# Optimization experiments

Hardware: AMD Instinct MI355X
Metric: run time of the kernel (lower is better)

The kernel has to match this reference:

```python
import jax, jax.numpy as jnp
import numpy as np

N_NODES = 200_000
N_EDGES = 400_000
EMB_DIM = 128
HID_DIM = 24
N_TYPES = 8


def setup_inputs() -> dict:
    key = jax.random.key(0)
    k_emb, k_src, k_typ, k_w1, k_w2 = jax.random.split(key, 5)
    rgcn_emb = jax.random.normal(k_emb, (N_NODES, EMB_DIM), dtype=jnp.float32)
    edge_index = jax.random.randint(k_src, (2, N_EDGES), 0, N_NODES, dtype=jnp.int32)
    edge_type = jax.random.randint(k_typ, (N_EDGES,), 0, N_TYPES, dtype=jnp.int32)
    # per-edge-type 2-layer MLP params: Linear(2D->H), Linear(H->1)
    W1 = jax.random.normal(k_w1, (N_TYPES, 2 * EMB_DIM, HID_DIM), dtype=jnp.float32) * 0.05
    b1 = jnp.zeros((N_TYPES, HID_DIM), dtype=jnp.float32)
    W2 = jax.random.normal(k_w2, (N_TYPES, HID_DIM), dtype=jnp.float32) * 0.05
    b2 = jnp.zeros((N_TYPES,), dtype=jnp.float32)
    return {"rgcn_emb": rgcn_emb, "edge_index": edge_index, "edge_type": edge_type,
            "W1": W1, "b1": b1, "W2": W2, "b2": b2}


def reference(rgcn_emb, edge_index, edge_type, W1, b1, W2, b2):
    src, dst = edge_index[0], edge_index[1]
    # gather + concat: [E, 2D]
    edge_emb = jnp.concatenate([rgcn_emb[src], rgcn_emb[dst]], axis=-1)
    # dense per-type expert compute, then select by routing (MoE-style)
    h = jnp.einsum('ed,tdh->teh', edge_emb, W1) + b1[:, None, :]  # [T,E,H]
    h = jnp.where(h > 0, h, 0.01 * h)  # LeakyReLU(0.01)
    s = jnp.einsum('teh,th->te', h, W2) + b2[:, None]  # [T,E]
    onehot = jax.nn.one_hot(edge_type, N_TYPES, dtype=s.dtype)  # [E,T]
    scores = jnp.einsum('te,et->e', s, onehot)  # scatter-select per edge
    return (scores, rgcn_emb)
```

## Files before the change

### kernel.cpp

```cpp
#include <hip/hip_runtime.h>


typedef _Float16 h2 __attribute__((ext_vector_type(2)));
typedef float    f4 __attribute__((ext_vector_type(4)));

constexpr int N_NODES = 200000;
constexpr int N_EDGES = 400000;
constexpr int EMB_DIM = 128;
constexpr int HID     = 24;
constexpr int N_TYPES = 8;
constexpr int BLK     = 256;

constexpr int MAX_PAD      = N_EDGES + N_TYPES * (BLK - 1);
constexpr int SCORE_BLOCKS = (MAX_PAD + BLK - 1) / BLK;
constexpr int SC_BLOCKS    = 128;
constexpr int SC_CH        = (N_EDGES + SC_BLOCKS - 1) / SC_BLOCKS;

constexpr int PREP_HIST   = 64;
constexpr int PREP_W1     = 16;
constexpr int PREP_CONV   = 1968;
constexpr int PREP_BLOCKS = PREP_HIST + PREP_W1 + PREP_CONV;

constexpr size_t SORT_BYTES  = (size_t)(16 + MAX_PAD) * sizeof(int);
constexpr size_t EMB16_OFF   = (SORT_BYTES + 255) & ~(size_t)255;
constexpr size_t EMB16_BYTES = (size_t)N_NODES * EMB_DIM * 2;
constexpr size_t W16_OFF     = EMB16_OFF + EMB16_BYTES;
constexpr size_t W16_BYTES   = (size_t)N_TYPES * 128 * HID * 4;
constexpr size_t NEED16      = W16_OFF + W16_BYTES;

__device__ __forceinline__ float fdot2f(h2 a, h2 b, float c) {
#if __has_builtin(__builtin_amdgcn_fdot2)
    return __builtin_amdgcn_fdot2(a, b, c, false);
#else
    return c + (float)a[0] * (float)b[0] + (float)a[1] * (float)b[1];
#endif
}

__global__ __launch_bounds__(BLK) void prep_k(
        const int* __restrict__ etype, int* __restrict__ counts,
        const float* __restrict__ emb, float* __restrict__ out,
        int2* __restrict__ emb16, const float* __restrict__ W1,
        h2* __restrict__ w16) {
    int b = blockIdx.x;
    if (b < PREP_HIST) {
        __shared__ int lc[N_TYPES];
        if (threadIdx.x < N_TYPES) lc[threadIdx.x] = 0;
        __syncthreads();
        const int4* et4 = (const int4*)etype;
        for (int g = b * BLK + threadIdx.x; g < N_EDGES / 4; g += PREP_HIST * BLK) {
            int4 v = et4[g];
            atomicAdd(&lc[v.x], 1); atomicAdd(&lc[v.y], 1);
            atomicAdd(&lc[v.z], 1); atomicAdd(&lc[v.w], 1);
        }
        __syncthreads();
        if (threadIdx.x < N_TYPES) {
            int v = lc[threadIdx.x];
            if (v) atomicAdd(&counts[threadIdx.x], v);
        }
    } else if (b < PREP_HIST + PREP_W1) {
        int cb = b - PREP_HIST;
        for (int p = cb * BLK + threadIdx.x; p < N_TYPES * 128 * HID; p += PREP_W1 * BLK) {
            int t   = p / (128 * HID);
            int rem = p - t * 128 * HID;
            int kp  = rem / HID, j = rem - kp * HID;
            h2 v;
            v[0] = (_Float16)W1[(t * 256 + 2 * kp)     * HID + j];
            v[1] = (_Float16)W1[(t * 256 + 2 * kp + 1) * HID + j];
            w16[p] = v;
        }
    } else {
        int cb = b - PREP_HIST - PREP_W1;
        const f4* in4 = (const f4*)emb;
        f4* o4 = (f4*)(out + N_EDGES);
        const int n4 = N_NODES * EMB_DIM / 4;
        for (int i = cb * BLK + threadIdx.x; i < n4; i += PREP_CONV * BLK) {
            f4 a = __builtin_nontemporal_load(&in4[i]);
            __builtin_nontemporal_store(a, &o4[i]);
            union { int2 v; h2 h[2]; } u;
            u.h[0] = h2{(_Float16)a.x, (_Float16)a.y};
            u.h[1] = h2{(_Float16)a.z, (_Float16)a.w};
            emb16[i] = u.v;
        }
    }
}

__global__ __launch_bounds__(BLK) void scatter_k(
        const int* __restrict__ etype, int* __restrict__ counts,
        int* __restrict__ sorted) {
    __shared__ int lc[N_TYPES], base[N_TYPES];
    int b = blockIdx.x;
    if (threadIdx.x < N_TYPES) lc[threadIdx.x] = 0;
    __syncthreads();
    int e0 = b * SC_CH, e1 = min(e0 + SC_CH, N_EDGES);
    for (int e = e0 + threadIdx.x; e < e1; e += BLK)
        atomicAdd(&lc[etype[e]], 1);
    __syncthreads();
    if (threadIdx.x < N_TYPES)
        base[threadIdx.x] = atomicAdd(&counts[8 + threadIdx.x], lc[threadIdx.x]);
    __syncthreads();
    if (threadIdx.x < N_TYPES) lc[threadIdx.x] = 0;
    __syncthreads();
    int poff[N_TYPES];
    int off = 0;
#pragma unroll
    for (int t = 0; t < N_TYPES; ++t) {
        poff[t] = off;
        off += ((counts[t] + BLK - 1) / BLK) * BLK;
    }
    for (int e = e0 + threadIdx.x; e < e1; e += BLK) {
        int t = etype[e];
        int r = atomicAdd(&lc[t], 1);
        sorted[poff[t] + base[t] + r] = e;
    }
}

__device__ __forceinline__ void compute_chunk(const int4* __restrict__ r,
                                              const h2* __restrict__ wrow,
                                              float acc[HID]) {
    const h2* hp = (const h2*)r;
#pragma unroll
    for (int kp = 0; kp < 32; ++kp) {
#pragma unroll
        for (int j = 0; j < HID; ++j)
            acc[j] = fdot2f(hp[kp], wrow[kp * HID + j], acc[j]);
    }
}

__global__ __launch_bounds__(BLK) void score16_ns_k(
        const unsigned short* __restrict__ emb16u,
        const int* __restrict__ srci, const int* __restrict__ dsti,
        const int* __restrict__ counts, const int* __restrict__ sorted,
        const h2* __restrict__ w16, const float* __restrict__ b1,
        const float* __restrict__ W2, const float* __restrict__ b2,
        float* __restrict__ out) {
    int poff[N_TYPES];
    int off = 0;
#pragma unroll
    for (int t = 0; t < N_TYPES; ++t) {
        poff[t] = off;
        off += ((counts[t] + BLK - 1) / BLK) * BLK;
    }
    int slot0 = blockIdx.x * BLK;
    if (slot0 >= off) return;
    int t = 0;
#pragma unroll
    for (int i = 1; i < N_TYPES; ++i)
        if (slot0 >= poff[i]) t = i;
    t = __builtin_amdgcn_readfirstlane(t);
    int cnt = counts[t];
    int local = slot0 - poff[t] + (int)threadIdx.x;
    if (local >= cnt) return;
    int e = sorted[slot0 + threadIdx.x];
    int s = srci[e], d = dsti[e];

    float acc[HID];
#pragma unroll
    for (int j = 0; j < HID; ++j) acc[j] = b1[t * HID + j];
    const h2* wt = w16 + (size_t)t * 128 * HID;
    const int4* x0 = (const int4*)(emb16u + (size_t)s * EMB_DIM);
    const int4* x1 = (const int4*)(emb16u + (size_t)d * EMB_DIM);

    int4 A[8], B[8];
#pragma unroll
    for (int k = 0; k < 8; ++k) A[k] = x0[k];
#pragma unroll
    for (int k = 0; k < 8; ++k) B[k] = x0[8 + k];
    compute_chunk(A, wt + 0 * 32 * HID, acc);
#pragma unroll
    for (int k = 0; k < 8; ++k) A[k] = x1[k];
    compute_chunk(B, wt + 1 * 32 * HID, acc);
#pragma unroll
    for (int k = 0; k < 8; ++k) B[k] = x1[8 + k];
    compute_chunk(A, wt + 2 * 32 * HID, acc);
    compute_chunk(B, wt + 3 * 32 * HID, acc);

    float sc = b2[t];
#pragma unroll
    for (int j = 0; j < HID; ++j) {
        float h = acc[j];
        h = (h > 0.f) ? h : 0.01f * h;
        sc = fmaf(h, W2[t * HID + j], sc);
    }
    out[e] = sc;
}

__global__ __launch_bounds__(BLK) void fallback_k(
        const float* __restrict__ emb,
        const int* __restrict__ srci, const int* __restrict__ dsti,
        const int* __restrict__ etype,
        const float* __restrict__ W1, const float* __restrict__ b1,
        const float* __restrict__ W2, const float* __restrict__ b2,
        float* __restrict__ out) {
    long long i0 = (long long)blockIdx.x * BLK + threadIdx.x;
    const float4* s4 = (const float4*)emb;
    float4* o4 = (float4*)(out + N_EDGES);
    const long long n4 = (long long)N_NODES * EMB_DIM / 4;
    for (long long i = i0; i < n4; i += (long long)gridDim.x * BLK)
        o4[i] = s4[i];
    for (int e = (int)i0; e < N_EDGES; e += gridDim.x * BLK) {
        int t = etype[e];
        int s = srci[e], d = dsti[e];
        float acc[HID];
#pragma unroll
        for (int j = 0; j < HID; ++j) acc[j] = b1[t * HID + j];
        const float* w = W1 + (size_t)t * 2 * EMB_DIM * HID;
        for (int k = 0; k < EMB_DIM; ++k) {
            float x = emb[(size_t)s * EMB_DIM + k];
#pragma unroll
            for (int j = 0; j < HID; ++j) acc[j] = fmaf(x, w[k * HID + j], acc[j]);
        }
        for (int k = 0; k < EMB_DIM; ++k) {
            float x = emb[(size_t)d * EMB_DIM + k];
#pragma unroll
            for (int j = 0; j < HID; ++j) acc[j] = fmaf(x, w[(EMB_DIM + k) * HID + j], acc[j]);
        }
        float sc = b2[t];
#pragma unroll
        for (int j = 0; j < HID; ++j) {
            float h = acc[j];
            h = (h > 0.f) ? h : 0.01f * h;
            sc = fmaf(h, W2[t * HID + j], sc);
        }
        out[e] = sc;
    }
}

extern "C" void kernel_launch(void* const* d_in, const int* in_sizes, int n_in,
                              void* d_out, int out_size, void* d_ws, size_t ws_size,
                              hipStream_t stream) {
    const float* emb   = (const float*)d_in[0];
    const int*   eidx  = (const int*)d_in[1];
    const int*   etype = (const int*)d_in[2];
    const float* W1    = (const float*)d_in[3];
    const float* b1    = (const float*)d_in[4];
    const float* W2    = (const float*)d_in[5];
    const float* b2    = (const float*)d_in[6];
    float* out = (float*)d_out;
    const int* srci = eidx;
    const int* dsti = eidx + N_EDGES;

    if (ws_size >= NEED16) {
        int* counts = (int*)d_ws;
        int* sorted = counts + 16;
        int2* emb16 = (int2*)((char*)d_ws + EMB16_OFF);
        h2*   w16   = (h2*)((char*)d_ws + W16_OFF);
        (void)hipMemsetAsync(counts, 0, 16 * sizeof(int), stream);
        prep_k<<<PREP_BLOCKS, BLK, 0, stream>>>(etype, counts, emb, out, emb16, W1, w16);
        scatter_k<<<SC_BLOCKS, BLK, 0, stream>>>(etype, counts, sorted);
        score16_ns_k<<<SCORE_BLOCKS, BLK, 0, stream>>>(
            (const unsigned short*)emb16, srci, dsti, counts, sorted,
            w16, b1, W2, b2, out);
    } else {
        fallback_k<<<2048, BLK, 0, stream>>>(emb, srci, dsti, etype, W1, b1, W2, b2, out);
    }
}
```

Baseline: 287.0 us.

## Replace multi-kernel pipeline with cooperative persistent megakernel and fp32 compute

Merges histogram, prefix, scatter and scoring into one cooperative kernel that uses grid syncs, and falls back to four separate launches if the cooperative launch fails. It drops the fp16 conversion of the embedding table and W1, so the per-edge MLP now reads fp32 embeddings and weights directly with fmaf. The memset goes away by replacing the atomic global counts with a per-chunk count table and a deterministic prefix sum. This saves launch overhead and the fp16 conversion pass, at the cost of twice the gather bandwidth per edge, fp32 math instead of dot2, and grid-sync latency.

```diff
diff --git a/kernel.cpp b/kernel.cpp
--- a/kernel.cpp
+++ b/kernel.cpp
@@ -1,8 +1,10 @@
 #include <hip/hip_runtime.h>
-
-
-typedef _Float16 h2 __attribute__((ext_vector_type(2)));
-typedef float    f4 __attribute__((ext_vector_type(4)));
+#include <hip/hip_cooperative_groups.h>
+
+
+namespace cg = cooperative_groups;
+
+typedef float f4 __attribute__((ext_vector_type(4)));
 
 constexpr int N_NODES = 200000;
 constexpr int N_EDGES = 400000;
@@ -11,178 +13,194 @@
 constexpr int N_TYPES = 8;
 constexpr int BLK     = 256;
 
-constexpr int MAX_PAD      = N_EDGES + N_TYPES * (BLK - 1);
+constexpr int CHUNKS  = 128;
+constexpr int CH_SZ   = N_EDGES / CHUNKS;
+constexpr int MAX_PAD = N_EDGES + N_TYPES * (BLK - 1);
 constexpr int SCORE_BLOCKS = (MAX_PAD + BLK - 1) / BLK;
-constexpr int SC_BLOCKS    = 128;
-constexpr int SC_CH        = (N_EDGES + SC_BLOCKS - 1) / SC_BLOCKS;
-
-constexpr int PREP_HIST   = 64;
-constexpr int PREP_W1     = 16;
-constexpr int PREP_CONV   = 1968;
-constexpr int PREP_BLOCKS = PREP_HIST + PREP_W1 + PREP_CONV;
-
-constexpr size_t SORT_BYTES  = (size_t)(16 + MAX_PAD) * sizeof(int);
-constexpr size_t EMB16_OFF   = (SORT_BYTES + 255) & ~(size_t)255;
-constexpr size_t EMB16_BYTES = (size_t)N_NODES * EMB_DIM * 2;
-constexpr size_t W16_OFF     = EMB16_OFF + EMB16_BYTES;
-constexpr size_t W16_BYTES   = (size_t)N_TYPES * 128 * HID * 4;
-constexpr size_t NEED16      = W16_OFF + W16_BYTES;
-
-__device__ __forceinline__ float fdot2f(h2 a, h2 b, float c) {
-#if __has_builtin(__builtin_amdgcn_fdot2)
-    return __builtin_amdgcn_fdot2(a, b, c, false);
-#else
-    return c + (float)a[0] * (float)b[0] + (float)a[1] * (float)b[1];
-#endif
-}
-
-__global__ __launch_bounds__(BLK) void prep_k(
-        const int* __restrict__ etype, int* __restrict__ counts,
-        const float* __restrict__ emb, float* __restrict__ out,
-        int2* __restrict__ emb16, const float* __restrict__ W1,
-        h2* __restrict__ w16) {
-    int b = blockIdx.x;
-    if (b < PREP_HIST) {
+
+constexpr int OFF_COUNTS = 0;
+constexpr int OFF_POFF   = 8;
+constexpr int OFF_CC     = 16;
+constexpr int OFF_BASE   = OFF_CC + CHUNKS * N_TYPES;
+constexpr int OFF_SORTED = OFF_BASE + CHUNKS * N_TYPES;
+constexpr size_t WS_INTS = (size_t)OFF_SORTED + MAX_PAD;
+
+
+__device__ __forceinline__ void phaseA(int b, int G,
+        const int* __restrict__ etype, const float* __restrict__ emb,
+        float* __restrict__ out, int* __restrict__ ws) {
+    if (b < CHUNKS) {
         __shared__ int lc[N_TYPES];
         if (threadIdx.x < N_TYPES) lc[threadIdx.x] = 0;
         __syncthreads();
-        const int4* et4 = (const int4*)etype;
-        for (int g = b * BLK + threadIdx.x; g < N_EDGES / 4; g += PREP_HIST * BLK) {
-            int4 v = et4[g];
-            atomicAdd(&lc[v.x], 1); atomicAdd(&lc[v.y], 1);
-            atomicAdd(&lc[v.z], 1); atomicAdd(&lc[v.w], 1);
-        }
-        __syncthreads();
-        if (threadIdx.x < N_TYPES) {
-            int v = lc[threadIdx.x];
-            if (v) atomicAdd(&counts[threadIdx.x], v);
-        }
-    } else if (b < PREP_HIST + PREP_W1) {
-        int cb = b - PREP_HIST;
-        for (int p = cb * BLK + threadIdx.x; p < N_TYPES * 128 * HID; p += PREP_W1 * BLK) {
-            int t   = p / (128 * HID);
-            int rem = p - t * 128 * HID;
-            int kp  = rem / HID, j = rem - kp * HID;
-            h2 v;
-            v[0] = (_Float16)W1[(t * 256 + 2 * kp)     * HID + j];
-            v[1] = (_Float16)W1[(t * 256 + 2 * kp + 1) * HID + j];
-            w16[p] = v;
-        }
+        int e0 = b * CH_SZ;
+        for (int e = e0 + (int)threadIdx.x; e < e0 + CH_SZ; e += BLK)
+            atomicAdd(&lc[etype[e]], 1);
+        __syncthreads();
+        if (threadIdx.x < N_TYPES)
+            ws[OFF_CC + b * N_TYPES + threadIdx.x] = lc[threadIdx.x];
     } else {
-        int cb = b - PREP_HIST - PREP_W1;
         const f4* in4 = (const f4*)emb;
         f4* o4 = (f4*)(out + N_EDGES);
         const int n4 = N_NODES * EMB_DIM / 4;
-        for (int i = cb * BLK + threadIdx.x; i < n4; i += PREP_CONV * BLK) {
-            f4 a = __builtin_nontemporal_load(&in4[i]);
+        int nb = G - CHUNKS;
+        for (int i = (b - CHUNKS) * BLK + (int)threadIdx.x; i < n4; i += nb * BLK) {
+            f4 a = in4[i];
             __builtin_nontemporal_store(a, &o4[i]);
-            union { int2 v; h2 h[2]; } u;
-            u.h[0] = h2{(_Float16)a.x, (_Float16)a.y};
-            u.h[1] = h2{(_Float16)a.z, (_Float16)a.w};
-            emb16[i] = u.v;
-        }
-    }
-}
-
-__global__ __launch_bounds__(BLK) void scatter_k(
-        const int* __restrict__ etype, int* __restrict__ counts,
-        int* __restrict__ sorted) {
-    __shared__ int lc[N_TYPES], base[N_TYPES];
-    int b = blockIdx.x;
-    if (threadIdx.x < N_TYPES) lc[threadIdx.x] = 0;
-    __syncthreads();
-    int e0 = b * SC_CH, e1 = min(e0 + SC_CH, N_EDGES);
-    for (int e = e0 + threadIdx.x; e < e1; e += BLK)
-        atomicAdd(&lc[etype[e]], 1);
-    __syncthreads();
-    if (threadIdx.x < N_TYPES)
-        base[threadIdx.x] = atomicAdd(&counts[8 + threadIdx.x], lc[threadIdx.x]);
-    __syncthreads();
-    if (threadIdx.x < N_TYPES) lc[threadIdx.x] = 0;
-    __syncthreads();
+        }
+    }
+}
+
+__device__ __forceinline__ void phaseB(int b, int* __restrict__ ws) {
+    if (b == 0) {
+        if (threadIdx.x < N_TYPES) {
+            int t = threadIdx.x;
+            int s = 0;
+            for (int c = 0; c < CHUNKS; ++c) {
+                ws[OFF_BASE + c * N_TYPES + t] = s;
+                s += ws[OFF_CC + c * N_TYPES + t];
+            }
+            ws[OFF_COUNTS + t] = s;
+        }
+        __syncthreads();
+        if (threadIdx.x == 0) {
+            int off = 0;
+            for (int t = 0; t < N_TYPES; ++t) {
+                ws[OFF_POFF + t] = off;
+                off += ((ws[OFF_COUNTS + t] + BLK - 1) / BLK) * BLK;
+            }
+        }
+    }
+}
+
+__device__ __forceinline__ void phaseC(int b, const int* __restrict__ etype,
+                                       int* __restrict__ ws) {
+    if (b < CHUNKS) {
+        __shared__ int lc[N_TYPES];
+        __shared__ int pbase[N_TYPES];
+        if (threadIdx.x < N_TYPES) {
+            lc[threadIdx.x] = 0;
+            pbase[threadIdx.x] = ws[OFF_POFF + threadIdx.x]
+                               + ws[OFF_BASE + b * N_TYPES + threadIdx.x];
+        }
+        __syncthreads();
+        int e0 = b * CH_SZ;
+        int* sorted = ws + OFF_SORTED;
+        for (int e = e0 + (int)threadIdx.x; e < e0 + CH_SZ; e += BLK) {
+            int t = etype[e];
+            int r = atomicAdd(&lc[t], 1);
+            sorted[pbase[t] + r] = e;
+        }
+    }
+}
+
+__device__ __forceinline__ void half_mm(const f4* __restrict__ x4,
+                                        const float* __restrict__ w,
+                                        float acc[HID]) {
+#pragma unroll 1
+    for (int c = 0; c < 4; ++c) {
+        f4 r[8];
+#pragma unroll
+        for (int k = 0; k < 8; ++k) r[k] = x4[c * 8 + k];
+#pragma unroll
+        for (int k = 0; k < 8; ++k) {
+            const float* wp = w + (c * 32 + k * 4) * HID;
+#pragma unroll
+            for (int j = 0; j < HID; ++j) acc[j] = fmaf(r[k][0], wp[0 * HID + j], acc[j]);
+#pragma unroll
+            for (int j = 0; j < HID; ++j) acc[j] = fmaf(r[k][1], wp[1 * HID + j], acc[j]);
+#pragma unroll
+            for (int j = 0; j < HID; ++j) acc[j] = fmaf(r[k][2], wp[2 * HID + j], acc[j]);
+#pragma unroll
+            for (int j = 0; j < HID; ++j) acc[j] = fmaf(r[k][3], wp[3 * HID + j], acc[j]);
+        }
+    }
+}
+
+__device__ __forceinline__ void phaseD(const float* __restrict__ emb,
+        const int* __restrict__ srci, const int* __restrict__ dsti,
+        const float* __restrict__ W1, const float* __restrict__ b1,
+        const float* __restrict__ W2, const float* __restrict__ b2,
+        const int* __restrict__ ws, float* __restrict__ out, int G) {
     int poff[N_TYPES];
     int off = 0;
 #pragma unroll
     for (int t = 0; t < N_TYPES; ++t) {
         poff[t] = off;
-        off += ((counts[t] + BLK - 1) / BLK) * BLK;
-    }
-    for (int e = e0 + threadIdx.x; e < e1; e += BLK) {
-        int t = etype[e];
-        int r = atomicAdd(&lc[t], 1);
-        sorted[poff[t] + base[t] + r] = e;
-    }
-}
-
-__device__ __forceinline__ void compute_chunk(const int4* __restrict__ r,
-                                              const h2* __restrict__ wrow,
-                                              float acc[HID]) {
-    const h2* hp = (const h2*)r;
-#pragma unroll
-    for (int kp = 0; kp < 32; ++kp) {
-#pragma unroll
-        for (int j = 0; j < HID; ++j)
-            acc[j] = fdot2f(hp[kp], wrow[kp * HID + j], acc[j]);
-    }
-}
-
-__global__ __launch_bounds__(BLK) void score16_ns_k(
-        const unsigned short* __restrict__ emb16u,
+        off += ((ws[OFF_COUNTS + t] + BLK - 1) / BLK) * BLK;
+    }
+    const int* sorted = ws + OFF_SORTED;
+    for (int wb = (int)blockIdx.x; wb * BLK < off; wb += G) {
+        int slot0 = wb * BLK;
+        int t = 0;
+#pragma unroll
+        for (int i = 1; i < N_TYPES; ++i)
+            if (slot0 >= poff[i]) t = i;
+        t = __builtin_amdgcn_readfirstlane(t);
+        int cnt = ws[OFF_COUNTS + t];
+        int local = slot0 - poff[t] + (int)threadIdx.x;
+        if (local < cnt) {
+            int e = sorted[slot0 + threadIdx.x];
+            int s = srci[e], d = dsti[e];
+            float acc[HID];
+#pragma unroll
+            for (int j = 0; j < HID; ++j) acc[j] = b1[t * HID + j];
+            const float* W1t = W1 + (size_t)t * (2 * EMB_DIM * HID);
+            half_mm((const f4*)(emb + (size_t)s * EMB_DIM), W1t, acc);
+            half_mm((const f4*)(emb + (size_t)d * EMB_DIM), W1t + EMB_DIM * HID, acc);
+            float sc = b2[t];
+#pragma unroll
+            for (int j = 0; j < HID; ++j) {
+                float h = acc[j];
+                h = (h > 0.f) ? h : 0.01f * h;
+                sc = fmaf(h, W2[t * HID + j], sc);
+            }
+            out[e] = sc;
+        }
+    }
+}
+
+
+__global__ __launch_bounds__(BLK, 7) void mega_k(
+        const float* __restrict__ emb, const int* __restrict__ srci,
+        const int* __restrict__ dsti, const int* __restrict__ etype,
+        const float* __restrict__ W1, const float* __restrict__ b1,
+        const float* __restrict__ W2, const float* __restrict__ b2,
+        float* __restrict__ out, int* __restrict__ ws) {
+    cg::grid_group grid = cg::this_grid();
+    int G = (int)gridDim.x;
+    phaseA((int)blockIdx.x, G, etype, emb, out, ws);
+    __threadfence();
+    grid.sync();
+    phaseB((int)blockIdx.x, ws);
+    __threadfence();
+    grid.sync();
+    phaseC((int)blockIdx.x, etype, ws);
+    __threadfence();
+    grid.sync();
+    phaseD(emb, srci, dsti, W1, b1, W2, b2, ws, out, G);
+}
+
+
+__global__ __launch_bounds__(BLK) void fa_k(const int* __restrict__ etype,
+        const float* __restrict__ emb, float* __restrict__ out, int* __restrict__ ws) {
+    phaseA((int)blockIdx.x, (int)gridDim.x, etype, emb, out, ws);
+}
+__global__ __launch_bounds__(BLK) void fb_k(int* __restrict__ ws) {
+    phaseB((int)blockIdx.x, ws);
+}
+__global__ __launch_bounds__(BLK) void fc_k(const int* __restrict__ etype,
+                                            int* __restrict__ ws) {
+    phaseC((int)blockIdx.x, etype, ws);
+}
+__global__ __launch_bounds__(BLK) void fd_k(const float* __restrict__ emb,
         const int* __restrict__ srci, const int* __restrict__ dsti,
-        const int* __restrict__ counts, const int* __restrict__ sorted,
-        const h2* __restrict__ w16, const float* __restrict__ b1,
-        const float* __restrict__ W2, const float* __restrict__ b2,
-        float* __restrict__ out) {
-    int poff[N_TYPES];
-    int off = 0;
-#pragma unroll
-    for (int t = 0; t < N_TYPES; ++t) {
-        poff[t] = off;
-        off += ((counts[t] + BLK - 1) / BLK) * BLK;
-    }
-    int slot0 = blockIdx.x * BLK;
-    if (slot0 >= off) return;
-    int t = 0;
-#pragma unroll
-    for (int i = 1; i < N_TYPES; ++i)
-        if (slot0 >= poff[i]) t = i;
-    t = __builtin_amdgcn_readfirstlane(t);
-    int cnt = counts[t];
-    int local = slot0 - poff[t] + (int)threadIdx.x;
-    if (local >= cnt) return;
-    int e = sorted[slot0 + threadIdx.x];
-    int s = srci[e], d = dsti[e];
-
-    float acc[HID];
-#pragma unroll
-    for (int j = 0; j < HID; ++j) acc[j] = b1[t * HID + j];
-    const h2* wt = w16 + (size_t)t * 128 * HID;
-    const int4* x0 = (const int4*)(emb16u + (size_t)s * EMB_DIM);
-    const int4* x1 = (const int4*)(emb16u + (size_t)d * EMB_DIM);
-
-    int4 A[8], B[8];
-#pragma unroll
-    for (int k = 0; k < 8; ++k) A[k] = x0[k];
-#pragma unroll
-    for (int k = 0; k < 8; ++k) B[k] = x0[8 + k];
-    compute_chunk(A, wt + 0 * 32 * HID, acc);
-#pragma unroll
-    for (int k = 0; k < 8; ++k) A[k] = x1[k];
-    compute_chunk(B, wt + 1 * 32 * HID, acc);
-#pragma unroll
-    for (int k = 0; k < 8; ++k) B[k] = x1[8 + k];
-    compute_chunk(A, wt + 2 * 32 * HID, acc);
-    compute_chunk(B, wt + 3 * 32 * HID, acc);
-
-    float sc = b2[t];
-#pragma unroll
-    for (int j = 0; j < HID; ++j) {
-        float h = acc[j];
-        h = (h > 0.f) ? h : 0.01f * h;
-        sc = fmaf(h, W2[t * HID + j], sc);
-    }
-    out[e] = sc;
-}
+        const float* __restrict__ W1, const float* __restrict__ b1,
+        const float* __restrict__ W2, const float* __restrict__ b2,
+        const int* __restrict__ ws, float* __restrict__ out) {
+    phaseD(emb, srci, dsti, W1, b1, W2, b2, ws, out, (int)gridDim.x);
+}
+
 
 __global__ __launch_bounds__(BLK) void fallback_k(
         const float* __restrict__ emb,
@@ -192,8 +210,8 @@
         const float* __restrict__ W2, const float* __restrict__ b2,
         float* __restrict__ out) {
     long long i0 = (long long)blockIdx.x * BLK + threadIdx.x;
-    const float4* s4 = (const float4*)emb;
-    float4* o4 = (float4*)(out + N_EDGES);
+    const f4* s4 = (const f4*)emb;
+    f4* o4 = (f4*)(out + N_EDGES);
     const long long n4 = (long long)N_NODES * EMB_DIM / 4;
     for (long long i = i0; i < n4; i += (long long)gridDim.x * BLK)
         o4[i] = s4[i];
@@ -204,16 +222,8 @@
 #pragma unroll
         for (int j = 0; j < HID; ++j) acc[j] = b1[t * HID + j];
         const float* w = W1 + (size_t)t * 2 * EMB_DIM * HID;
-        for (int k = 0; k < EMB_DIM; ++k) {
-            float x = emb[(size_t)s * EMB_DIM + k];
-#pragma unroll
-            for (int j = 0; j < HID; ++j) acc[j] = fmaf(x, w[k * HID + j], acc[j]);
-        }
-        for (int k = 0; k < EMB_DIM; ++k) {
-            float x = emb[(size_t)d * EMB_DIM + k];
-#pragma unroll
-            for (int j = 0; j < HID; ++j) acc[j] = fmaf(x, w[(EMB_DIM + k) * HID + j], acc[j]);
-        }
+        half_mm((const f4*)(emb + (size_t)s * EMB_DIM), w, acc);
+        half_mm((const f4*)(emb + (size_t)d * EMB_DIM), w + EMB_DIM * HID, acc);
         float sc = b2[t];
 #pragma unroll
         for (int j = 0; j < HID; ++j) {
@@ -239,17 +249,31 @@
     const int* srci = eidx;
     const int* dsti = eidx + N_EDGES;
 
-    if (ws_size >= NEED16) {
-        int* counts = (int*)d_ws;
-        int* sorted = counts + 16;
-        int2* emb16 = (int2*)((char*)d_ws + EMB16_OFF);
-        h2*   w16   = (h2*)((char*)d_ws + W16_OFF);
-        (void)hipMemsetAsync(counts, 0, 16 * sizeof(int), stream);
-        prep_k<<<PREP_BLOCKS, BLK, 0, stream>>>(etype, counts, emb, out, emb16, W1, w16);
-        scatter_k<<<SC_BLOCKS, BLK, 0, stream>>>(etype, counts, sorted);
-        score16_ns_k<<<SCORE_BLOCKS, BLK, 0, stream>>>(
-            (const unsigned short*)emb16, srci, dsti, counts, sorted,
-            w16, b1, W2, b2, out);
+    if (ws_size >= WS_INTS * sizeof(int)) {
+        int* ws = (int*)d_ws;
+        int nb = 0;
+        hipError_t oe = hipOccupancyMaxActiveBlocksPerMultiprocessor(
+            &nb, (const void*)mega_k, BLK, 0);
+        int G = 0;
+        if (oe == hipSuccess && nb > 0) {
+            G = nb * 256;
+            if (G > 2048) G = 2048;
+        }
+        bool launched = false;
+        if (G >= CHUNKS + 8) {
+            void* args[] = {(void*)&emb, (void*)&srci, (void*)&dsti, (void*)&etype,
+                            (void*)&W1, (void*)&b1, (void*)&W2, (void*)&b2,
+                            (void*)&out, (void*)&ws};
+            hipError_t le = hipLaunchCooperativeKernel(
+                (const void*)mega_k, dim3(G), dim3(BLK), args, 0, stream);
+            launched = (le == hipSuccess);
+        }
+        if (!launched) {
+            fa_k<<<1792, BLK, 0, stream>>>(etype, emb, out, ws);
+            fb_k<<<1, BLK, 0, stream>>>(ws);
+            fc_k<<<CHUNKS, BLK, 0, stream>>>(etype, ws);
+            fd_k<<<SCORE_BLOCKS, BLK, 0, stream>>>(emb, srci, dsti, W1, b1, W2, b2, ws, out);
+        }
     } else {
         fallback_k<<<2048, BLK, 0, stream>>>(emb, srci, dsti, etype, W1, b1, W2, b2, out);
     }
```

Measured after the change: 802.5 us. 180% more time.
